# Performance work log

Hardware: AMD Instinct MI355X
Metric: run time of the kernel (lower is better)

## Reference

```python
import jax, jax.numpy as jnp
import numpy as np

N_EMBD = 2048
N_Q = 32
N_KV = 8
GROUP = N_Q // N_KV   # 4
HD = N_EMBD // N_Q    # 64
BASE = 10000.0
NEG_INF = -1e30


def _rope(x):
    """Rotate-half RoPE on last dim; positions 1..t along dim -2 (as in the
    original _build_cache which uses arange(1, seq_len+1))."""
    t, d = x.shape[-2], x.shape[-1]
    d2 = d // 2
    theta = 1.0 / (BASE ** (jnp.arange(0, d, 2, dtype=jnp.float32) / d))  # (d/2,)
    pos = jnp.arange(1, t + 1, dtype=jnp.float32)                          # (t,)
    ang = pos[:, None] * theta[None, :]                                    # (t, d/2)
    ang = jnp.concatenate([ang, ang], axis=-1)                             # (t, d)
    sin, cos = jnp.sin(ang), jnp.cos(ang)
    rot = jnp.concatenate([-x[..., d2:], x[..., :d2]], axis=-1)
    return x * cos + rot * sin


def setup_inputs() -> dict:
    key = jax.random.key(0)
    ks = jax.random.split(key, 5)
    b, t = 2, 1024
    s = 1.0 / np.sqrt(N_EMBD)
    return {
        "x": jax.random.normal(ks[0], (b, t, N_EMBD), dtype=jnp.float32),
        "wq": jax.random.normal(ks[1], (N_EMBD, N_EMBD), dtype=jnp.float32) * s,
        "bq": jnp.zeros((N_EMBD,), dtype=jnp.float32),
        "wk": jax.random.normal(ks[2], (N_EMBD, N_KV * HD), dtype=jnp.float32) * s,
        "bk": jnp.zeros((N_KV * HD,), dtype=jnp.float32),
        "wv": jax.random.normal(ks[3], (N_EMBD, N_KV * HD), dtype=jnp.float32) * s,
        "bv": jnp.zeros((N_KV * HD,), dtype=jnp.float32),
        "wo": jax.random.normal(ks[4], (N_EMBD, N_EMBD), dtype=jnp.float32) * s,
        "bo": jnp.zeros((N_EMBD,), dtype=jnp.float32),
    }


def reference(x, wq, bq, wk, bk, wv, bv, wo, bo):
    b, t, _ = x.shape
    q = x @ wq + bq                                   # (b, t, E)
    k = x @ wk + bk                                   # (b, t, NKV*HD)
    v = x @ wv + bv
    q = q.reshape(b, t, N_Q, HD).transpose(0, 2, 1, 3)        # (b, nq, t, d)
    q = q.reshape(b, N_KV, GROUP, t, HD)                      # (b, hkv, g, t, d)
    k = k.reshape(b, t, N_KV, HD).transpose(0, 2, 1, 3)       # (b, hkv, t, d)
    v = v.reshape(b, t, N_KV, HD).transpose(0, 2, 1, 3)
    q = _rope(q)
    k = _rope(k)
    scale = jnp.sqrt(jnp.float32(HD))
    att = jnp.einsum("bhgqd,bhkd->bhgqk", q, k) / scale       # (b, hkv, g, t, t)
    causal = jnp.tril(jnp.ones((t, t), dtype=bool))
    att = jnp.where(causal, att, NEG_INF)
    att = jax.nn.softmax(att, axis=-1)
    out = jnp.einsum("bhgqk,bhkd->bhgqd", att, v)             # (b, hkv, g, t, d)
    out = out.transpose(0, 3, 1, 2, 4).reshape(b, t, N_EMBD)  # (b, t, E)
    return out @ wo + bo
```

## Files before the change

kernel.cpp:

```cpp
#include <hip/hip_runtime.h>
#include <hip/hip_bf16.h>
#include <cstdint>


typedef __attribute__((ext_vector_type(8))) short short8;
typedef __attribute__((ext_vector_type(4))) short short4v;
typedef __attribute__((ext_vector_type(4))) float f32x4;

__device__ inline short f2b(float f) {
  union { float f; unsigned u; } v; v.f = f;
  unsigned r = v.u + 0x7fffu + ((v.u >> 16) & 1u);
  return (short)(r >> 16);
}

__device__ inline float exp2_fast(float x) {
  float r;
  asm("v_exp_f32 %0, %1" : "=v"(r) : "v"(x));
  return r;
}

__device__ inline void gl_lds16(const void* g, void* l) {
  __builtin_amdgcn_global_load_lds((const __attribute__((address_space(1))) void*)g,
                                   (__attribute__((address_space(3))) void*)l,
                                   16, 0, 0);
}

__global__ void cast_x_kernel(const float* __restrict__ x, short* __restrict__ xb, int n4) {
  int i = blockIdx.x * 256 + threadIdx.x;
  if (i >= n4) return;
  float4 v = ((const float4*)x)[i];
  short4v o; o.x = f2b(v.x); o.y = f2b(v.y); o.z = f2b(v.z); o.w = f2b(v.w);
  ((short4v*)xb)[i] = o;
}

__global__ void wtrans_all(const float* __restrict__ wq, const float* __restrict__ wk,
                           const float* __restrict__ wv, const float* __restrict__ wo,
                           short* __restrict__ WqkvT, short* __restrict__ woT) {
  __shared__ float tile[64][65];
  const int bx = blockIdx.x;
  const float* W; short* WT; int N, off, nb;
  if (bx < 32)      { W = wq; WT = WqkvT; N = 2048; off = 0;    nb = bx * 64; }
  else if (bx < 40) { W = wk; WT = WqkvT; N = 512;  off = 2048; nb = (bx - 32) * 64; }
  else if (bx < 48) { W = wv; WT = WqkvT; N = 512;  off = 2560; nb = (bx - 40) * 64; }
  else              { W = wo; WT = woT;   N = 2048; off = 0;    nb = (bx - 48) * 64; }
  const int kb = blockIdx.y * 64;
  const int tid = threadIdx.x;
  const int c = tid & 63, r0 = tid >> 6;
#pragma unroll
  for (int s = 0; s < 16; ++s) {
    int k = r0 + s * 4;
    tile[c][k] = W[(size_t)(kb + k) * N + nb + c];
  }
  __syncthreads();
#pragma unroll
  for (int s = 0; s < 16; ++s) {
    int n = r0 + s * 4;
    WT[(size_t)(off + nb + n) * 2048 + kb + c] = f2b(tile[n][c]);
  }
}

__device__ __forceinline__ void gemm_loop_bk64(const short* __restrict__ Ag,
                                               const short* __restrict__ Bg,
                                               short* lA, short* lB,
                                               int w, int l15, int q4,
                                               f32x4 acc[2][4]) {
  const int K = 2048, NS = 32;
  auto stage = [&](int s, int d) {
    const short* As = Ag + s * 64;
    const short* Bs = Bg + s * 64;
    short* a = lA + d * 8192 + w * 512;
    gl_lds16(As, a);
    gl_lds16(As + 64 * K, a + 2048);
    gl_lds16(As + 32, a + 4096);
    gl_lds16(As + 64 * K + 32, a + 6144);
    short* bp = lB + d * 4096 + w * 512;
    gl_lds16(Bs, bp);
    gl_lds16(Bs + 32, bp + 2048);
  };
  stage(0, 0);
  for (int s = 0; s < NS; ++s) {
    const int d = s & 1;
    __syncthreads();
    if (s + 1 < NS) stage(s + 1, d ^ 1);
#pragma unroll
    for (int ks = 0; ks < 2; ++ks) {
      const short* ap = lA + d * 8192 + ks * 4096;
      const short* bp = lB + d * 4096 + ks * 2048;
      short8 af[2], bf[4];
#pragma unroll
      for (int mf = 0; mf < 2; ++mf) af[mf] = *(const short8*)(ap + (w * 32 + mf * 16 + l15) * 32 + q4 * 8);
#pragma unroll
      for (int nf = 0; nf < 4; ++nf) bf[nf] = *(const short8*)(bp + (nf * 16 + l15) * 32 + q4 * 8);
#pragma unroll
      for (int mf = 0; mf < 2; ++mf)
#pragma unroll
        for (int nf = 0; nf < 4; ++nf)
          acc[mf][nf] = __builtin_amdgcn_mfma_f32_16x16x32_bf16(af[mf], bf[nf], acc[mf][nf], 0, 0, 0);
    }
  }
}

__launch_bounds__(256, 3)
__global__ void gemm_qkv(const short* __restrict__ A, const short* __restrict__ BT,
                         const float* __restrict__ bq, const float* __restrict__ bk,
                         const float* __restrict__ bv,
                         short* __restrict__ Qb, short* __restrict__ Kb,
                         short* __restrict__ Vtd) {
  __shared__ __align__(16) short lA[16384];
  __shared__ __align__(16) short lB[8192];
  const int K = 2048;
  const int tid = threadIdx.x, lane = tid & 63, w = tid >> 6;
  const int q4 = lane >> 4, l15 = lane & 15;
  const int bn = blockIdx.x * 64, bm = blockIdx.y * 128;

  const short* Ag = A + (size_t)(bm + (tid >> 2)) * K + ((tid & 3) << 3);
  const short* Bg = BT + (size_t)(bn + (tid >> 2)) * K + ((tid & 3) << 3);

  f32x4 acc[2][4];
  const f32x4 fz = {0.f, 0.f, 0.f, 0.f};
#pragma unroll
  for (int i = 0; i < 2; ++i)
#pragma unroll
    for (int j = 0; j < 4; ++j) acc[i][j] = fz;

  gemm_loop_bk64(Ag, Bg, lA, lB, w, l15, q4, acc);

  const float L2T = 0.4152410118609203f;
  const float theta_a = exp2_fast(-(float)l15 * L2T);
  const float theta_b = exp2_fast(-(float)(l15 + 16) * L2T);
  const float s2 = 0.18033688011112042f;

  if (bn < 2048) {
    const int h = bn >> 6;
    float bb0 = bq[bn + l15], bb1 = bq[bn + 16 + l15], bb2 = bq[bn + 32 + l15], bb3 = bq[bn + 48 + l15];
#pragma unroll
    for (int mf = 0; mf < 2; ++mf)
#pragma unroll
      for (int r = 0; r < 4; ++r) {
        int row = bm + w * 32 + mf * 16 + q4 * 4 + r;
        int batch = row >> 10, t = row & 1023;
        float pos = (float)(t + 1);
        float sa, ca, sb, cb;
        __sincosf(pos * theta_a, &sa, &ca);
        __sincosf(pos * theta_b, &sb, &cb);
        float x0 = acc[mf][0][r] + bb0, x2 = acc[mf][2][r] + bb2;
        float x1 = acc[mf][1][r] + bb1, x3 = acc[mf][3][r] + bb3;
        size_t base = ((size_t)(batch * 32 + h) * 1024 + t) * 64;
        Qb[base + l15]      = f2b((x0 * ca - x2 * sa) * s2);
        Qb[base + l15 + 32] = f2b((x2 * ca + x0 * sa) * s2);
        Qb[base + l15 + 16] = f2b((x1 * cb - x3 * sb) * s2);
        Qb[base + l15 + 48] = f2b((x3 * cb + x1 * sb) * s2);
      }
  } else if (bn < 2560) {
    const int co = bn - 2048;
    const int hkv = co >> 6;
    float bb0 = bk[co + l15], bb1 = bk[co + 16 + l15], bb2 = bk[co + 32 + l15], bb3 = bk[co + 48 + l15];
#pragma unroll
    for (int mf = 0; mf < 2; ++mf)
#pragma unroll
      for (int r = 0; r < 4; ++r) {
        int row = bm + w * 32 + mf * 16 + q4 * 4 + r;
        int batch = row >> 10, t = row & 1023;
        float pos = (float)(t + 1);
        float sa, ca, sb, cb;
        __sincosf(pos * theta_a, &sa, &ca);
        __sincosf(pos * theta_b, &sb, &cb);
        float x0 = acc[mf][0][r] + bb0, x2 = acc[mf][2][r] + bb2;
        float x1 = acc[mf][1][r] + bb1, x3 = acc[mf][3][r] + bb3;
        size_t base = (size_t)(batch * 8 + hkv) * 65536 + t * 32;
        Kb[base + l15]              = f2b(x0 * ca - x2 * sa);
        Kb[base + l15 + 16]         = f2b(x1 * cb - x3 * sb);
        Kb[base + 32768 + l15]      = f2b(x2 * ca + x0 * sa);
        Kb[base + 32768 + l15 + 16] = f2b(x3 * cb + x1 * sb);
      }
  } else {
    const int co = bn - 2560;
    const int hkv = co >> 6;
    float bb[4];
#pragma unroll
    for (int nf = 0; nf < 4; ++nf) bb[nf] = bv[co + nf * 16 + l15];
#pragma unroll
    for (int mf = 0; mf < 2; ++mf)
#pragma unroll
      for (int r = 0; r < 4; ++r) {
        int row = bm + w * 32 + mf * 16 + q4 * 4 + r;
        int batch = row >> 10, t = row & 1023;
        size_t base = (size_t)(batch * 8 + hkv) * 65536 + (size_t)t * 64;
#pragma unroll
        for (int nf = 0; nf < 4; ++nf)
          Vtd[base + nf * 16 + l15] = f2b(acc[mf][nf][r] + bb[nf]);
      }
  }
}

__global__ void vtrans2_kernel(const short* __restrict__ Vtd, short* __restrict__ VTb) {
  __shared__ short tile[64][72];
  const int tt = blockIdx.x, h = blockIdx.y, b = blockIdx.z;
  const int tid = threadIdx.x;
  const size_t base = (size_t)(b * 8 + h) * 65536;
#pragma unroll
  for (int p = 0; p < 2; ++p) {
    int r = (tid >> 3) + p * 32;
    int c0 = (tid & 7) * 8;
    short8 v = *(const short8*)(Vtd + base + (size_t)(tt * 64 + r) * 64 + c0);
#pragma unroll
    for (int j = 0; j < 8; ++j) tile[c0 + j][r] = v[j];
  }
  __syncthreads();
  const int d = tid >> 2, ts = (tid & 3) * 8;
#pragma unroll
  for (int tc = 0; tc < 2; ++tc) {
    short8 v = *(const short8*)(&tile[d][tc * 32 + ts]);
    *(short8*)(VTb + base + (size_t)(tt * 2 + tc) * 2048 + d * 32 + ts) = v;
  }
}

#define PROW 72
__launch_bounds__(256, 3)
__global__ void attn5_kernel(const short* __restrict__ Qb, const short* __restrict__ Kb,
                             const short* __restrict__ VTb, short* __restrict__ AO) {
  __shared__ __align__(16) short lK[2][128 * 32];
  __shared__ __align__(16) short lVT[4][64 * 32];
  __shared__ __align__(16) short lP[4][2][16 * PROW];
  const int tid = threadIdx.x, lane = tid & 63, w = tid >> 6;
  const int q4 = lane >> 4, l15 = lane & 15;
  const int qt = (int)gridDim.x - 1 - (int)blockIdx.x;
  const int h = blockIdx.y, b = blockIdx.z;
  const int hkv = h >> 2;
  const int qb = qt * 128 + w * 32;
  const int kdiag = qb >> 6;
  const int ns = qt + 1;

  const short* Qg = Qb + (size_t)(b * 32 + h) * 65536;
  const short* Kg = Kb + (size_t)(b * 8 + hkv) * 65536;
  const short* Vg = VTb + (size_t)(b * 8 + hkv) * 65536;

  short8 qf[2][2];
#pragma unroll
  for (int mf = 0; mf < 2; ++mf) {
    const short* qr = Qg + (size_t)(qb + mf * 16 + l15) * 64 + q4 * 8;
    qf[mf][0] = *(const short8*)(qr);
    qf[mf][1] = *(const short8*)(qr + 32);
  }

  const f32x4 fz = {0.f, 0.f, 0.f, 0.f};
  f32x4 o[2][4], ol[2];
#pragma unroll
  for (int mf = 0; mf < 2; ++mf) {
    ol[mf] = fz;
#pragma unroll
    for (int i = 0; i < 4; ++i) o[mf][i] = fz;
  }
  short8 ones;
#pragma unroll
  for (int i = 0; i < 8; ++i) ones[i] = (short)0x3F80;

  for (int s = 0; s < ns; ++s) {
    {
      const short* Ksrc = Kg + (size_t)(s * 128 + (tid >> 2)) * 32 + (tid & 3) * 8;
      short* ldst = (short*)lK + w * 512;
      gl_lds16(Ksrc, ldst);
      gl_lds16(Ksrc + 64 * 32, ldst + 2048);
      gl_lds16(Ksrc + 32768, ldst + 4096);
      gl_lds16(Ksrc + 32768 + 64 * 32, ldst + 6144);
      const short* Vsrc = Vg + (size_t)(s * 4) * 2048 + tid * 8;
      short* vdst = (short*)lVT + w * 512;
#pragma unroll
      for (int c = 0; c < 4; ++c) gl_lds16(Vsrc + c * 2048, vdst + c * 2048);
    }
    __syncthreads();

#pragma unroll
    for (int ki = 0; ki < 2; ++ki) {
      const int ktg = s * 2 + ki;
      if (ktg <= kdiag) {
        short8 kf0[4], kf1[4];
#pragma unroll
        for (int nt = 0; nt < 4; ++nt) {
          kf0[nt] = *(const short8*)((short*)lK + (ki * 64 + nt * 16 + l15) * 32 + q4 * 8);
          kf1[nt] = *(const short8*)((short*)lK + 4096 + (ki * 64 + nt * 16 + l15) * 32 + q4 * 8);
        }
        const bool diag = (ktg == kdiag);
#pragma unroll
        for (int mf = 0; mf < 2; ++mf) {
          f32x4 sv[4];
#pragma unroll
          for (int nt = 0; nt < 4; ++nt) {
            f32x4 z = __builtin_amdgcn_mfma_f32_16x16x32_bf16(qf[mf][0], kf0[nt], fz, 0, 0, 0);
            sv[nt] = __builtin_amdgcn_mfma_f32_16x16x32_bf16(qf[mf][1], kf1[nt], z, 0, 0, 0);
          }
          if (diag) {
#pragma unroll
            for (int r = 0; r < 4; ++r) {
              const int qrow = qb + mf * 16 + q4 * 4 + r;
              const int col = ktg * 64 + l15;
#pragma unroll
              for (int nt = 0; nt < 4; ++nt)
                if (col + nt * 16 > qrow) sv[nt][r] = -1e30f;
            }
          }
          short* lPm = lP[w][mf];
#pragma unroll
          for (int r = 0; r < 4; ++r)
#pragma unroll
            for (int nt = 0; nt < 4; ++nt)
              lPm[(q4 * 4 + r) * PROW + nt * 16 + l15] = f2b(exp2_fast(sv[nt][r] - 16.f));
        }

        short8 vf0[4], vf1[4];
#pragma unroll
        for (int dt = 0; dt < 4; ++dt) {
          vf0[dt] = *(const short8*)((short*)lVT + (2 * ki) * 2048 + (dt * 16 + l15) * 32 + q4 * 8);
          vf1[dt] = *(const short8*)((short*)lVT + (2 * ki + 1) * 2048 + (dt * 16 + l15) * 32 + q4 * 8);
        }
#pragma unroll
        for (int mf = 0; mf < 2; ++mf) {
          const short* lPm = lP[w][mf];
          short8 pf0 = *(const short8*)(lPm + l15 * PROW + q4 * 8);
          short8 pf1 = *(const short8*)(lPm + l15 * PROW + 32 + q4 * 8);
          ol[mf] = __builtin_amdgcn_mfma_f32_16x16x32_bf16(pf0, ones, ol[mf], 0, 0, 0);
          ol[mf] = __builtin_amdgcn_mfma_f32_16x16x32_bf16(pf1, ones, ol[mf], 0, 0, 0);
#pragma unroll
          for (int dt = 0; dt < 4; ++dt) {
            o[mf][dt] = __builtin_amdgcn_mfma_f32_16x16x32_bf16(pf0, vf0[dt], o[mf][dt], 0, 0, 0);
            o[mf][dt] = __builtin_amdgcn_mfma_f32_16x16x32_bf16(pf1, vf1[dt], o[mf][dt], 0, 0, 0);
          }
        }
      }
    }
    __syncthreads();
  }

#pragma unroll
  for (int mf = 0; mf < 2; ++mf)
#pragma unroll
    for (int r = 0; r < 4; ++r) {
      float inv = __builtin_amdgcn_rcpf(ol[mf][r]);
      int row = qb + mf * 16 + q4 * 4 + r;
#pragma unroll
      for (int dt = 0; dt < 4; ++dt)
        AO[(size_t)(b * 1024 + row) * 2048 + h * 64 + dt * 16 + l15] = f2b(o[mf][dt][r] * inv);
    }
}

__launch_bounds__(256, 3)
__global__ void gemm_out(const short* __restrict__ A, const short* __restrict__ BT,
                         float* __restrict__ C, const float* __restrict__ bias,
                         int N, int K) {
  __shared__ __align__(16) short lA[16384];
  __shared__ __align__(16) short lB[8192];
  const int tid = threadIdx.x, lane = tid & 63, w = tid >> 6;
  const int q4 = lane >> 4, l15 = lane & 15;
  const int bn = blockIdx.x * 64, bm = blockIdx.y * 128;

  const short* Ag = A + (size_t)(bm + (tid >> 2)) * K + ((tid & 3) << 3);
  const short* Bg = BT + (size_t)(bn + (tid >> 2)) * K + ((tid & 3) << 3);

  f32x4 acc[2][4];
  const f32x4 fz = {0.f, 0.f, 0.f, 0.f};
#pragma unroll
  for (int i = 0; i < 2; ++i)
#pragma unroll
    for (int j = 0; j < 4; ++j) acc[i][j] = fz;

  gemm_loop_bk64(Ag, Bg, lA, lB, w, l15, q4, acc);

#pragma unroll
  for (int mf = 0; mf < 2; ++mf)
#pragma unroll
    for (int nf = 0; nf < 4; ++nf) {
      int col = bn + nf * 16 + l15;
      float bb = bias[col];
#pragma unroll
      for (int r = 0; r < 4; ++r) {
        int row = bm + w * 32 + mf * 16 + q4 * 4 + r;
        C[(size_t)row * N + col] = acc[mf][nf][r] + bb;
      }
    }
}

extern "C" void kernel_launch(void* const* d_in, const int* in_sizes, int n_in,
                              void* d_out, int out_size, void* d_ws, size_t ws_size,
                              hipStream_t stream) {
  const float* x  = (const float*)d_in[0];
  const float* wq = (const float*)d_in[1];
  const float* bq = (const float*)d_in[2];
  const float* wk = (const float*)d_in[3];
  const float* bk = (const float*)d_in[4];
  const float* wv = (const float*)d_in[5];
  const float* bv = (const float*)d_in[6];
  const float* wo = (const float*)d_in[7];
  const float* bo = (const float*)d_in[8];
  float* out = (float*)d_out;
  const int B = in_sizes[0] / (1024 * 2048);
  const int M = B * 1024;

  char* ws = (char*)d_ws;
  size_t off = 0;
  auto alloc = [&](size_t bytes) -> char* {
    char* p = ws + off;
    off += (bytes + 255) & ~(size_t)255;
    return p;
  };
  short* xb    = (short*)alloc((size_t)M * 2048 * 2);
  short* WqkvT = (short*)alloc((size_t)3072 * 2048 * 2);
  short* woT   = (short*)alloc((size_t)2048 * 2048 * 2);
  short* Qb    = (short*)alloc((size_t)B * 32 * 1024 * 64 * 2);
  short* Kb    = (short*)alloc((size_t)B * 8 * 2 * 1024 * 32 * 2);
  short* Vtd   = (short*)alloc((size_t)B * 8 * 1024 * 64 * 2);
  short* VTb   = (short*)alloc((size_t)B * 8 * 32 * 64 * 32 * 2);
  short* AO    = (short*)alloc((size_t)M * 2048 * 2);

  cast_x_kernel<<<(M * 2048 / 4 + 255) / 256, 256, 0, stream>>>(x, xb, M * 2048 / 4);
  wtrans_all<<<dim3(80, 32), 256, 0, stream>>>(wq, wk, wv, wo, WqkvT, woT);
  gemm_qkv<<<dim3(48, M / 128), 256, 0, stream>>>(xb, WqkvT, bq, bk, bv, Qb, Kb, Vtd);
  vtrans2_kernel<<<dim3(16, 8, B), 256, 0, stream>>>(Vtd, VTb);
  attn5_kernel<<<dim3(8, 32, B), 256, 0, stream>>>(Qb, Kb, VTb, AO);
  gemm_out<<<dim3(32, M / 128), 256, 0, stream>>>(AO, woT, out, bo, 2048, 2048);
}
```

Baseline: 208.7 us.

## Swizzle LDS layouts and deepen GEMM pipeline to four-stage half-tile ring

The GEMM main loop moves from a double-buffered BK=64 schedule to a four-slot ring of BK=32 half-steps with three loads in flight. Each step waits with explicit vmcnt counts and a raw s_barrier instead of __syncthreads, and MFMA priority is raised with s_setprio. The source column offsets of the global-to-LDS copies and the fragment read offsets are XOR-swizzled in both the GEMMs and the attention kernel, to cut LDS bank conflicts on the short8 reads. The hand-counted vmcnt values and the swizzle must match the copy pattern exactly, or the results go wrong.

New measurement: 226.3 us. 8.4% more time.

```diff
diff --git a/kernel.cpp b/kernel.cpp
--- a/kernel.cpp
+++ b/kernel.cpp
@@ -64,40 +64,59 @@
                                                short* lA, short* lB,
                                                int w, int l15, int q4,
                                                f32x4 acc[2][4]) {
-  const int K = 2048, NS = 32;
-  auto stage = [&](int s, int d) {
-    const short* As = Ag + s * 64;
-    const short* Bs = Bg + s * 64;
-    short* a = lA + d * 8192 + w * 512;
+  const int K = 2048, HS = 64;
+  const int q4x = q4 ^ ((l15 >> 1) & 3);
+
+  auto issue = [&](int h) {
+    const short* As = Ag + h * 32;
+    const short* Bs = Bg + h * 32;
+    const int be = h & 3;
+    short* a = lA + be * 4096 + w * 512;
     gl_lds16(As, a);
     gl_lds16(As + 64 * K, a + 2048);
-    gl_lds16(As + 32, a + 4096);
-    gl_lds16(As + 64 * K + 32, a + 6144);
-    short* bp = lB + d * 4096 + w * 512;
-    gl_lds16(Bs, bp);
-    gl_lds16(Bs + 32, bp + 2048);
+    gl_lds16(Bs, lB + be * 2048 + w * 512);
   };
-  stage(0, 0);
-  for (int s = 0; s < NS; ++s) {
-    const int d = s & 1;
-    __syncthreads();
-    if (s + 1 < NS) stage(s + 1, d ^ 1);
-#pragma unroll
-    for (int ks = 0; ks < 2; ++ks) {
-      const short* ap = lA + d * 8192 + ks * 4096;
-      const short* bp = lB + d * 4096 + ks * 2048;
-      short8 af[2], bf[4];
-#pragma unroll
-      for (int mf = 0; mf < 2; ++mf) af[mf] = *(const short8*)(ap + (w * 32 + mf * 16 + l15) * 32 + q4 * 8);
-#pragma unroll
-      for (int nf = 0; nf < 4; ++nf) bf[nf] = *(const short8*)(bp + (nf * 16 + l15) * 32 + q4 * 8);
-#pragma unroll
-      for (int mf = 0; mf < 2; ++mf)
-#pragma unroll
-        for (int nf = 0; nf < 4; ++nf)
-          acc[mf][nf] = __builtin_amdgcn_mfma_f32_16x16x32_bf16(af[mf], bf[nf], acc[mf][nf], 0, 0, 0);
-    }
-  }
+  auto halfstep = [&](int h) {
+    const int be = h & 3;
+    const short* ap = lA + be * 4096;
+    const short* bp = lB + be * 2048;
+    short8 af[2], bf[4];
+#pragma unroll
+    for (int mf = 0; mf < 2; ++mf)
+      af[mf] = *(const short8*)(ap + (w * 32 + mf * 16 + l15) * 32 + q4x * 8);
+#pragma unroll
+    for (int nf = 0; nf < 4; ++nf)
+      bf[nf] = *(const short8*)(bp + (nf * 16 + l15) * 32 + q4x * 8);
+    __builtin_amdgcn_s_setprio(1);
+#pragma unroll
+    for (int mf = 0; mf < 2; ++mf)
+#pragma unroll
+      for (int nf = 0; nf < 4; ++nf)
+        acc[mf][nf] = __builtin_amdgcn_mfma_f32_16x16x32_bf16(af[mf], bf[nf], acc[mf][nf], 0, 0, 0);
+    __builtin_amdgcn_s_setprio(0);
+  };
+
+  issue(0); issue(1); issue(2);
+  for (int h = 0; h < HS - 3; ++h) {
+    asm volatile("s_waitcnt vmcnt(6)" ::: "memory");
+    __builtin_amdgcn_s_barrier();
+    asm volatile("" ::: "memory");
+    __builtin_amdgcn_sched_barrier(0);
+    issue(h + 3);
+    halfstep(h);
+  }
+  asm volatile("s_waitcnt vmcnt(6)" ::: "memory");
+  __builtin_amdgcn_s_barrier();
+  asm volatile("" ::: "memory");
+  halfstep(HS - 3);
+  asm volatile("s_waitcnt vmcnt(3)" ::: "memory");
+  __builtin_amdgcn_s_barrier();
+  asm volatile("" ::: "memory");
+  halfstep(HS - 2);
+  asm volatile("s_waitcnt vmcnt(0)" ::: "memory");
+  __builtin_amdgcn_s_barrier();
+  asm volatile("" ::: "memory");
+  halfstep(HS - 1);
 }
 
 __launch_bounds__(256, 3)
@@ -113,8 +132,9 @@
   const int q4 = lane >> 4, l15 = lane & 15;
   const int bn = blockIdx.x * 64, bm = blockIdx.y * 128;
 
-  const short* Ag = A + (size_t)(bm + (tid >> 2)) * K + ((tid & 3) << 3);
-  const short* Bg = BT + (size_t)(bn + (tid >> 2)) * K + ((tid & 3) << 3);
+  const int swzc = ((tid & 3) ^ ((tid >> 3) & 3)) << 3;
+  const short* Ag = A + (size_t)(bm + (tid >> 2)) * K + swzc;
+  const short* Bg = BT + (size_t)(bn + (tid >> 2)) * K + swzc;
 
   f32x4 acc[2][4];
   const f32x4 fz = {0.f, 0.f, 0.f, 0.f};
@@ -224,6 +244,8 @@
   __shared__ __align__(16) short lP[4][2][16 * PROW];
   const int tid = threadIdx.x, lane = tid & 63, w = tid >> 6;
   const int q4 = lane >> 4, l15 = lane & 15;
+  const int q4x = q4 ^ ((l15 >> 1) & 3);
+  const int swzc = ((tid & 3) ^ ((tid >> 3) & 3)) << 3;
   const int qt = (int)gridDim.x - 1 - (int)blockIdx.x;
   const int h = blockIdx.y, b = blockIdx.z;
   const int hkv = h >> 2;
@@ -257,13 +279,13 @@
 
   for (int s = 0; s < ns; ++s) {
     {
-      const short* Ksrc = Kg + (size_t)(s * 128 + (tid >> 2)) * 32 + (tid & 3) * 8;
+      const short* Ksrc = Kg + (size_t)(s * 128 + (tid >> 2)) * 32 + swzc;
       short* ldst = (short*)lK + w * 512;
       gl_lds16(Ksrc, ldst);
       gl_lds16(Ksrc + 64 * 32, ldst + 2048);
       gl_lds16(Ksrc + 32768, ldst + 4096);
       gl_lds16(Ksrc + 32768 + 64 * 32, ldst + 6144);
-      const short* Vsrc = Vg + (size_t)(s * 4) * 2048 + tid * 8;
+      const short* Vsrc = Vg + (size_t)(s * 4) * 2048 + (tid >> 2) * 32 + swzc;
       short* vdst = (short*)lVT + w * 512;
 #pragma unroll
       for (int c = 0; c < 4; ++c) gl_lds16(Vsrc + c * 2048, vdst + c * 2048);
@@ -277,8 +299,8 @@
         short8 kf0[4], kf1[4];
 #pragma unroll
         for (int nt = 0; nt < 4; ++nt) {
-          kf0[nt] = *(const short8*)((short*)lK + (ki * 64 + nt * 16 + l15) * 32 + q4 * 8);
-          kf1[nt] = *(const short8*)((short*)lK + 4096 + (ki * 64 + nt * 16 + l15) * 32 + q4 * 8);
+          kf0[nt] = *(const short8*)((short*)lK + (ki * 64 + nt * 16 + l15) * 32 + q4x * 8);
+          kf1[nt] = *(const short8*)((short*)lK + 4096 + (ki * 64 + nt * 16 + l15) * 32 + q4x * 8);
         }
         const bool diag = (ktg == kdiag);
 #pragma unroll
@@ -310,8 +332,8 @@
         short8 vf0[4], vf1[4];
 #pragma unroll
         for (int dt = 0; dt < 4; ++dt) {
-          vf0[dt] = *(const short8*)((short*)lVT + (2 * ki) * 2048 + (dt * 16 + l15) * 32 + q4 * 8);
-          vf1[dt] = *(const short8*)((short*)lVT + (2 * ki + 1) * 2048 + (dt * 16 + l15) * 32 + q4 * 8);
+          vf0[dt] = *(const short8*)((short*)lVT + (2 * ki) * 2048 + (dt * 16 + l15) * 32 + q4x * 8);
+          vf1[dt] = *(const short8*)((short*)lVT + (2 * ki + 1) * 2048 + (dt * 16 + l15) * 32 + q4x * 8);
         }
 #pragma unroll
         for (int mf = 0; mf < 2; ++mf) {
@@ -353,8 +375,9 @@
   const int q4 = lane >> 4, l15 = lane & 15;
   const int bn = blockIdx.x * 64, bm = blockIdx.y * 128;
 
-  const short* Ag = A + (size_t)(bm + (tid >> 2)) * K + ((tid & 3) << 3);
-  const short* Bg = BT + (size_t)(bn + (tid >> 2)) * K + ((tid & 3) << 3);
+  const int swzc = ((tid & 3) ^ ((tid >> 3) & 3)) << 3;
+  const short* Ag = A + (size_t)(bm + (tid >> 2)) * K + swzc;
+  const short* Bg = BT + (size_t)(bn + (tid >> 2)) * K + swzc;
 
   f32x4 acc[2][4];
   const f32x4 fz = {0.f, 0.f, 0.f, 0.f};
```

## Use 128x128 GEMM tiles with 2x2 wave layout and XOR-swizzled LDS

Applied to the files above, without the earlier changes.

The QKV and output projection GEMMs move from 128x64 tiles with BK=64 to 128x128 tiles with BK=32. Each wave now computes a 64x64 sub-tile, which raises arithmetic intensity and halves the number of blocks. An XOR swizzle on the 16-byte column chunk is applied to both the global-to-LDS loads and the fragment reads, in the GEMMs and in the attention K/V tiles, to cut LDS bank conflicts. The cost is more accumulator registers, fewer blocks (grids of 24x16 and 16x16 on a large GPU, so lower occupancy), and twice as many K-loop iterations with a barrier each.

Result: slower. 225.7 us (+8.1%).

```diff
diff --git a/kernel.cpp b/kernel.cpp
--- a/kernel.cpp
+++ b/kernel.cpp
@@ -59,44 +59,42 @@
   }
 }
 
-__device__ __forceinline__ void gemm_loop_bk64(const short* __restrict__ Ag,
-                                               const short* __restrict__ Bg,
-                                               short* lA, short* lB,
-                                               int w, int l15, int q4,
-                                               f32x4 acc[2][4]) {
-  const int K = 2048, NS = 32;
+__device__ __forceinline__ void gemm_loop_128(const short* __restrict__ Ag,
+                                              const short* __restrict__ Bg,
+                                              short* lA, short* lB,
+                                              int w, int wr, int wc, int l15, int q4,
+                                              f32x4 acc[4][4]) {
+  const int K = 2048, NS = 64;
+  const int q4x = q4 ^ ((l15 >> 1) & 3);
+
   auto stage = [&](int s, int d) {
-    const short* As = Ag + s * 64;
-    const short* Bs = Bg + s * 64;
-    short* a = lA + d * 8192 + w * 512;
-    gl_lds16(As, a);
-    gl_lds16(As + 64 * K, a + 2048);
-    gl_lds16(As + 32, a + 4096);
-    gl_lds16(As + 64 * K + 32, a + 6144);
-    short* bp = lB + d * 4096 + w * 512;
-    gl_lds16(Bs, bp);
-    gl_lds16(Bs + 32, bp + 2048);
+    const short* As = Ag + s * 32;
+    const short* Bs = Bg + s * 32;
+    gl_lds16(As,          lA + d * 4096 + w * 512);
+    gl_lds16(As + 64 * K, lA + d * 4096 + 2048 + w * 512);
+    gl_lds16(Bs,          lB + d * 4096 + w * 512);
+    gl_lds16(Bs + 64 * K, lB + d * 4096 + 2048 + w * 512);
   };
+
   stage(0, 0);
   for (int s = 0; s < NS; ++s) {
     const int d = s & 1;
     __syncthreads();
     if (s + 1 < NS) stage(s + 1, d ^ 1);
-#pragma unroll
-    for (int ks = 0; ks < 2; ++ks) {
-      const short* ap = lA + d * 8192 + ks * 4096;
-      const short* bp = lB + d * 4096 + ks * 2048;
-      short8 af[2], bf[4];
-#pragma unroll
-      for (int mf = 0; mf < 2; ++mf) af[mf] = *(const short8*)(ap + (w * 32 + mf * 16 + l15) * 32 + q4 * 8);
-#pragma unroll
-      for (int nf = 0; nf < 4; ++nf) bf[nf] = *(const short8*)(bp + (nf * 16 + l15) * 32 + q4 * 8);
-#pragma unroll
-      for (int mf = 0; mf < 2; ++mf)
-#pragma unroll
-        for (int nf = 0; nf < 4; ++nf)
-          acc[mf][nf] = __builtin_amdgcn_mfma_f32_16x16x32_bf16(af[mf], bf[nf], acc[mf][nf], 0, 0, 0);
-    }
+    const short* ap = lA + d * 4096;
+    const short* bp = lB + d * 4096;
+    short8 af[4], bf[4];
+#pragma unroll
+    for (int mi = 0; mi < 4; ++mi)
+      af[mi] = *(const short8*)(ap + (wr * 64 + mi * 16 + l15) * 32 + q4x * 8);
+#pragma unroll
+    for (int ni = 0; ni < 4; ++ni)
+      bf[ni] = *(const short8*)(bp + (wc * 64 + ni * 16 + l15) * 32 + q4x * 8);
+#pragma unroll
+    for (int mi = 0; mi < 4; ++mi)
+#pragma unroll
+      for (int ni = 0; ni < 4; ++ni)
+        acc[mi][ni] = __builtin_amdgcn_mfma_f32_16x16x32_bf16(af[mi], bf[ni], acc[mi][ni], 0, 0, 0);
   }
 }
 
@@ -106,89 +104,92 @@
                          const float* __restrict__ bv,
                          short* __restrict__ Qb, short* __restrict__ Kb,
                          short* __restrict__ Vtd) {
-  __shared__ __align__(16) short lA[16384];
+  __shared__ __align__(16) short lA[8192];
   __shared__ __align__(16) short lB[8192];
   const int K = 2048;
   const int tid = threadIdx.x, lane = tid & 63, w = tid >> 6;
+  const int wr = w >> 1, wc = w & 1;
   const int q4 = lane >> 4, l15 = lane & 15;
-  const int bn = blockIdx.x * 64, bm = blockIdx.y * 128;
-
-  const short* Ag = A + (size_t)(bm + (tid >> 2)) * K + ((tid & 3) << 3);
-  const short* Bg = BT + (size_t)(bn + (tid >> 2)) * K + ((tid & 3) << 3);
-
-  f32x4 acc[2][4];
+  const int bn = blockIdx.x * 128, bm = blockIdx.y * 128;
+
+  const int swzc = ((tid & 3) ^ ((tid >> 3) & 3)) << 3;
+  const short* Ag = A + (size_t)(bm + (tid >> 2)) * K + swzc;
+  const short* Bg = BT + (size_t)(bn + (tid >> 2)) * K + swzc;
+
+  f32x4 acc[4][4];
   const f32x4 fz = {0.f, 0.f, 0.f, 0.f};
 #pragma unroll
-  for (int i = 0; i < 2; ++i)
+  for (int i = 0; i < 4; ++i)
 #pragma unroll
     for (int j = 0; j < 4; ++j) acc[i][j] = fz;
 
-  gemm_loop_bk64(Ag, Bg, lA, lB, w, l15, q4, acc);
+  gemm_loop_128(Ag, Bg, lA, lB, w, wr, wc, l15, q4, acc);
 
   const float L2T = 0.4152410118609203f;
   const float theta_a = exp2_fast(-(float)l15 * L2T);
   const float theta_b = exp2_fast(-(float)(l15 + 16) * L2T);
   const float s2 = 0.18033688011112042f;
-
-  if (bn < 2048) {
-    const int h = bn >> 6;
-    float bb0 = bq[bn + l15], bb1 = bq[bn + 16 + l15], bb2 = bq[bn + 32 + l15], bb3 = bq[bn + 48 + l15];
-#pragma unroll
-    for (int mf = 0; mf < 2; ++mf)
+  const int cb = bn + wc * 64;
+
+  if (cb < 2048) {
+    const int h = cb >> 6;
+    float bb0 = bq[cb + l15], bb1 = bq[cb + 16 + l15], bb2 = bq[cb + 32 + l15], bb3 = bq[cb + 48 + l15];
+#pragma unroll
+    for (int mi = 0; mi < 4; ++mi)
 #pragma unroll
       for (int r = 0; r < 4; ++r) {
-        int row = bm + w * 32 + mf * 16 + q4 * 4 + r;
+        int row = bm + wr * 64 + mi * 16 + q4 * 4 + r;
         int batch = row >> 10, t = row & 1023;
         float pos = (float)(t + 1);
-        float sa, ca, sb, cb;
+        float sa, ca, sb, cb2;
         __sincosf(pos * theta_a, &sa, &ca);
-        __sincosf(pos * theta_b, &sb, &cb);
-        float x0 = acc[mf][0][r] + bb0, x2 = acc[mf][2][r] + bb2;
-        float x1 = acc[mf][1][r] + bb1, x3 = acc[mf][3][r] + bb3;
+        __sincosf(pos * theta_b, &sb, &cb2);
+        float x0 = acc[mi][0][r] + bb0, x2 = acc[mi][2][r] + bb2;
+        float x1 = acc[mi][1][r] + bb1, x3 = acc[mi][3][r] + bb3;
         size_t base = ((size_t)(batch * 32 + h) * 1024 + t) * 64;
         Qb[base + l15]      = f2b((x0 * ca - x2 * sa) * s2);
         Qb[base + l15 + 32] = f2b((x2 * ca + x0 * sa) * s2);
-        Qb[base + l15 + 16] = f2b((x1 * cb - x3 * sb) * s2);
-        Qb[base + l15 + 48] = f2b((x3 * cb + x1 * sb) * s2);
+        Qb[base + l15 + 16] = f2b((x1 * cb2 - x3 * sb) * s2);
+        Qb[base + l15 + 48] = f2b((x3 * cb2 + x1 * sb) * s2);
       }
-  } else if (bn < 2560) {
-    const int co = bn - 2048;
+  } else if (cb < 2560) {
+    const int co = cb - 2048;
     const int hkv = co >> 6;
     float bb0 = bk[co + l15], bb1 = bk[co + 16 + l15], bb2 = bk[co + 32 + l15], bb3 = bk[co + 48 + l15];
 #pragma unroll
-    for (int mf = 0; mf < 2; ++mf)
+    for (int mi = 0; mi < 4; ++mi)
 #pragma unroll
       for (int r = 0; r < 4; ++r) {
-        int row = bm + w * 32 + mf * 16 + q4 * 4 + r;
+        int row = bm + wr * 64 + mi * 16 + q4 * 4 + r;
         int batch = row >> 10, t = row & 1023;
         float pos = (float)(t + 1);
-        float sa, ca, sb, cb;
+        float sa, ca, sb, cb2;
         __sincosf(pos * theta_a, &sa, &ca);
-        __sincosf(pos * theta_b, &sb, &cb);
-        float x0 = acc[mf][0][r] + bb0, x2 = acc[mf][2][r] + bb2;
-        float x1 = acc[mf][1][r] + bb1, x3 = acc[mf][3][r] + bb3;
+        __sincosf(pos * theta_b, &sb, &cb2);
+        float x0 = acc[mi][0][r] + bb0, x2 = acc[mi][2][r] + bb2;
+        float x1 = acc[mi][1][r] + bb1, x3 = acc[mi][3][r] + bb3;
         size_t base = (size_t)(batch * 8 + hkv) * 65536 + t * 32;
         Kb[base + l15]              = f2b(x0 * ca - x2 * sa);
-        Kb[base + l15 + 16]         = f2b(x1 * cb - x3 * sb);
+        Kb[base + l15 + 16]         = f2b(x1 * cb2 - x3 * sb);
         Kb[base + 32768 + l15]      = f2b(x2 * ca + x0 * sa);
-        Kb[base + 32768 + l15 + 16] = f2b(x3 * cb + x1 * sb);
+        Kb[base + 32768 + l15 + 16] = f2b(x3 * cb2 + x1 * sb);
       }
   } else {
-    const int co = bn - 2560;
+    const int co = cb - 2560;
     const int hkv = co >> 6;
     float bb[4];
 #pragma unroll
     for (int nf = 0; nf < 4; ++nf) bb[nf] = bv[co + nf * 16 + l15];
 #pragma unroll
-    for (int mf = 0; mf < 2; ++mf)
+    for (int mi = 0; mi < 4; ++mi)
 #pragma unroll
       for (int r = 0; r < 4; ++r) {
-        int row = bm + w * 32 + mf * 16 + q4 * 4 + r;
+        int row = bm + wr * 64 + mi * 16 + q4 * 4 + r;
         int batch = row >> 10, t = row & 1023;
         size_t base = (size_t)(batch * 8 + hkv) * 65536 + (size_t)t * 64;
 #pragma unroll
         for (int nf = 0; nf < 4; ++nf)
-          Vtd[base + nf * 16 + l15] = f2b(acc[mf][nf][r] + bb[nf]);
+          Vtd[base + nf * 16 + l15] = f2b(acc[mi][nf][r] + bb[nf]);
       }
   }
 }
@@ -224,6 +225,8 @@
   __shared__ __align__(16) short lP[4][2][16 * PROW];
   const int tid = threadIdx.x, lane = tid & 63, w = tid >> 6;
   const int q4 = lane >> 4, l15 = lane & 15;
+  const int q4x = q4 ^ ((l15 >> 1) & 3);
+  const int swzc = ((tid & 3) ^ ((tid >> 3) & 3)) << 3;
   const int qt = (int)gridDim.x - 1 - (int)blockIdx.x;
   const int h = blockIdx.y, b = blockIdx.z;
   const int hkv = h >> 2;
@@ -257,13 +260,13 @@
 
   for (int s = 0; s < ns; ++s) {
     {
-      const short* Ksrc = Kg + (size_t)(s * 128 + (tid >> 2)) * 32 + (tid & 3) * 8;
+      const short* Ksrc = Kg + (size_t)(s * 128 + (tid >> 2)) * 32 + swzc;
       short* ldst = (short*)lK + w * 512;
       gl_lds16(Ksrc, ldst);
       gl_lds16(Ksrc + 64 * 32, ldst + 2048);
       gl_lds16(Ksrc + 32768, ldst + 4096);
       gl_lds16(Ksrc + 32768 + 64 * 32, ldst + 6144);
-      const short* Vsrc = Vg + (size_t)(s * 4) * 2048 + tid * 8;
+      const short* Vsrc = Vg + (size_t)(s * 4) * 2048 + (tid >> 2) * 32 + swzc;
       short* vdst = (short*)lVT + w * 512;
 #pragma unroll
       for (int c = 0; c < 4; ++c) gl_lds16(Vsrc + c * 2048, vdst + c * 2048);
@@ -277,8 +280,8 @@
         short8 kf0[4], kf1[4];
 #pragma unroll
         for (int nt = 0; nt < 4; ++nt) {
-          kf0[nt] = *(const short8*)((short*)lK + (ki * 64 + nt * 16 + l15) * 32 + q4 * 8);
-          kf1[nt] = *(const short8*)((short*)lK + 4096 + (ki * 64 + nt * 16 + l15) * 32 + q4 * 8);
+          kf0[nt] = *(const short8*)((short*)lK + (ki * 64 + nt * 16 + l15) * 32 + q4x * 8);
+          kf1[nt] = *(const short8*)((short*)lK + 4096 + (ki * 64 + nt * 16 + l15) * 32 + q4x * 8);
         }
         const bool diag = (ktg == kdiag);
 #pragma unroll
@@ -310,8 +313,8 @@
         short8 vf0[4], vf1[4];
 #pragma unroll
         for (int dt = 0; dt < 4; ++dt) {
-          vf0[dt] = *(const short8*)((short*)lVT + (2 * ki) * 2048 + (dt * 16 + l15) * 32 + q4 * 8);
-          vf1[dt] = *(const short8*)((short*)lVT + (2 * ki + 1) * 2048 + (dt * 16 + l15) * 32 + q4 * 8);
+          vf0[dt] = *(const short8*)((short*)lVT + (2 * ki) * 2048 + (dt * 16 + l15) * 32 + q4x * 8);
+          vf1[dt] = *(const short8*)((short*)lVT + (2 * ki + 1) * 2048 + (dt * 16 + l15) * 32 + q4x * 8);
         }
 #pragma unroll
         for (int mf = 0; mf < 2; ++mf) {
@@ -347,34 +350,36 @@
 __global__ void gemm_out(const short* __restrict__ A, const short* __restrict__ BT,
                          float* __restrict__ C, const float* __restrict__ bias,
                          int N, int K) {
-  __shared__ __align__(16) short lA[16384];
+  __shared__ __align__(16) short lA[8192];
   __shared__ __align__(16) short lB[8192];
   const int tid = threadIdx.x, lane = tid & 63, w = tid >> 6;
+  const int wr = w >> 1, wc = w & 1;
   const int q4 = lane >> 4, l15 = lane & 15;
-  const int bn = blockIdx.x * 64, bm = blockIdx.y * 128;
-
-  const short* Ag = A + (size_t)(bm + (tid >> 2)) * K + ((tid & 3) << 3);
-  const short* Bg = BT + (size_t)(bn + (tid >> 2)) * K + ((tid & 3) << 3);
-
-  f32x4 acc[2][4];
+  const int bn = blockIdx.x * 128, bm = blockIdx.y * 128;
+
+  const int swzc = ((tid & 3) ^ ((tid >> 3) & 3)) << 3;
+  const short* Ag = A + (size_t)(bm + (tid >> 2)) * K + swzc;
+  const short* Bg = BT + (size_t)(bn + (tid >> 2)) * K + swzc;
+
+  f32x4 acc[4][4];
   const f32x4 fz = {0.f, 0.f, 0.f, 0.f};
 #pragma unroll
-  for (int i = 0; i < 2; ++i)
+  for (int i = 0; i < 4; ++i)
 #pragma unroll
     for (int j = 0; j < 4; ++j) acc[i][j] = fz;
 
-  gemm_loop_bk64(Ag, Bg, lA, lB, w, l15, q4, acc);
-
-#pragma unroll
-  for (int mf = 0; mf < 2; ++mf)
-#pragma unroll
-    for (int nf = 0; nf < 4; ++nf) {
-      int col = bn + nf * 16 + l15;
+  gemm_loop_128(Ag, Bg, lA, lB, w, wr, wc, l15, q4, acc);
+
+#pragma unroll
+  for (int mi = 0; mi < 4; ++mi)
+#pragma unroll
+    for (int ni = 0; ni < 4; ++ni) {
+      int col = bn + wc * 64 + ni * 16 + l15;
       float bb = bias[col];
 #pragma unroll
       for (int r = 0; r < 4; ++r) {
-        int row = bm + w * 32 + mf * 16 + q4 * 4 + r;
-        C[(size_t)row * N + col] = acc[mf][nf][r] + bb;
+        int row = bm + wr * 64 + mi * 16 + q4 * 4 + r;
+        C[(size_t)row * N + col] = acc[mi][ni][r] + bb;
       }
     }
 }
@@ -413,8 +418,8 @@
 
   cast_x_kernel<<<(M * 2048 / 4 + 255) / 256, 256, 0, stream>>>(x, xb, M * 2048 / 4);
   wtrans_all<<<dim3(80, 32), 256, 0, stream>>>(wq, wk, wv, wo, WqkvT, woT);
-  gemm_qkv<<<dim3(48, M / 128), 256, 0, stream>>>(xb, WqkvT, bq, bk, bv, Qb, Kb, Vtd);
+  gemm_qkv<<<dim3(24, M / 128), 256, 0, stream>>>(xb, WqkvT, bq, bk, bv, Qb, Kb, Vtd);
   vtrans2_kernel<<<dim3(16, 8, B), 256, 0, stream>>>(Vtd, VTb);
   attn5_kernel<<<dim3(8, 32, B), 256, 0, stream>>>(Qb, Kb, VTb, AO);
-  gemm_out<<<dim3(32, M / 128), 256, 0, stream>>>(AO, woT, out, bo, 2048, 2048);
-}
+  gemm_out<<<dim3(16, M / 128), 256, 0, stream>>>(AO, woT, out, bo, 2048, 2048);
+}
```

## Swizzle LDS tiles to avoid bank conflicts and fuse V transpose into QKV GEMM

Applied to the files above, without the earlier changes.

Applies an XOR swizzle to the 16-byte chunk index both when global-to-LDS loads write tiles and when MFMA fragments are read back, in the GEMM loop and the attention kernel. This is meant to cut LDS bank conflicts on the fragment reads. The QKV GEMM epilogue now writes V straight into the transposed blocked layout that attention consumes, as packed 4-element stores, so the separate vtrans2 kernel and its intermediate buffer go away. The cost is slightly more index arithmetic and less coalesced V stores.

New measurement: 206.2 us. About the same (-1.2%).

```diff
diff --git a/kernel.cpp b/kernel.cpp
--- a/kernel.cpp
+++ b/kernel.cpp
@@ -65,6 +65,7 @@
                                                int w, int l15, int q4,
                                                f32x4 acc[2][4]) {
   const int K = 2048, NS = 32;
+  const int q4x = q4 ^ ((l15 >> 1) & 3);
   auto stage = [&](int s, int d) {
     const short* As = Ag + s * 64;
     const short* Bs = Bg + s * 64;
@@ -88,9 +89,9 @@
       const short* bp = lB + d * 4096 + ks * 2048;
       short8 af[2], bf[4];
 #pragma unroll
-      for (int mf = 0; mf < 2; ++mf) af[mf] = *(const short8*)(ap + (w * 32 + mf * 16 + l15) * 32 + q4 * 8);
-#pragma unroll
-      for (int nf = 0; nf < 4; ++nf) bf[nf] = *(const short8*)(bp + (nf * 16 + l15) * 32 + q4 * 8);
+      for (int mf = 0; mf < 2; ++mf) af[mf] = *(const short8*)(ap + (w * 32 + mf * 16 + l15) * 32 + q4x * 8);
+#pragma unroll
+      for (int nf = 0; nf < 4; ++nf) bf[nf] = *(const short8*)(bp + (nf * 16 + l15) * 32 + q4x * 8);
 #pragma unroll
       for (int mf = 0; mf < 2; ++mf)
 #pragma unroll
@@ -105,7 +106,7 @@
                          const float* __restrict__ bq, const float* __restrict__ bk,
                          const float* __restrict__ bv,
                          short* __restrict__ Qb, short* __restrict__ Kb,
-                         short* __restrict__ Vtd) {
+                         short* __restrict__ VTb) {
   __shared__ __align__(16) short lA[16384];
   __shared__ __align__(16) short lB[8192];
   const int K = 2048;
@@ -113,8 +114,9 @@
   const int q4 = lane >> 4, l15 = lane & 15;
   const int bn = blockIdx.x * 64, bm = blockIdx.y * 128;
 
-  const short* Ag = A + (size_t)(bm + (tid >> 2)) * K + ((tid & 3) << 3);
-  const short* Bg = BT + (size_t)(bn + (tid >> 2)) * K + ((tid & 3) << 3);
+  const int swzc = ((tid & 3) ^ ((tid >> 3) & 3)) << 3;
+  const short* Ag = A + (size_t)(bm + (tid >> 2)) * K + swzc;
+  const short* Bg = BT + (size_t)(bn + (tid >> 2)) * K + swzc;
 
   f32x4 acc[2][4];
   const f32x4 fz = {0.f, 0.f, 0.f, 0.f};
@@ -179,39 +181,20 @@
     float bb[4];
 #pragma unroll
     for (int nf = 0; nf < 4; ++nf) bb[nf] = bv[co + nf * 16 + l15];
-#pragma unroll
-    for (int mf = 0; mf < 2; ++mf)
-#pragma unroll
-      for (int r = 0; r < 4; ++r) {
-        int row = bm + w * 32 + mf * 16 + q4 * 4 + r;
-        int batch = row >> 10, t = row & 1023;
-        size_t base = (size_t)(batch * 8 + hkv) * 65536 + (size_t)t * 64;
-#pragma unroll
-        for (int nf = 0; nf < 4; ++nf)
-          Vtd[base + nf * 16 + l15] = f2b(acc[mf][nf][r] + bb[nf]);
+    const int batch = (bm + w * 32) >> 10;
+    const size_t vbase = (size_t)(batch * 8 + hkv) * 65536;
+#pragma unroll
+    for (int mf = 0; mf < 2; ++mf) {
+      const int t0 = (bm + w * 32 + mf * 16 + q4 * 4) & 1023;
+      const size_t rbase = vbase + (size_t)(t0 >> 5) * 2048 + (t0 & 31);
+#pragma unroll
+      for (int nf = 0; nf < 4; ++nf) {
+        short4v pk;
+#pragma unroll
+        for (int r = 0; r < 4; ++r) pk[r] = f2b(acc[mf][nf][r] + bb[nf]);
+        *(short4v*)(VTb + rbase + (nf * 16 + l15) * 32) = pk;
       }
-  }
-}
-
-__global__ void vtrans2_kernel(const short* __restrict__ Vtd, short* __restrict__ VTb) {
-  __shared__ short tile[64][72];
-  const int tt = blockIdx.x, h = blockIdx.y, b = blockIdx.z;
-  const int tid = threadIdx.x;
-  const size_t base = (size_t)(b * 8 + h) * 65536;
-#pragma unroll
-  for (int p = 0; p < 2; ++p) {
-    int r = (tid >> 3) + p * 32;
-    int c0 = (tid & 7) * 8;
-    short8 v = *(const short8*)(Vtd + base + (size_t)(tt * 64 + r) * 64 + c0);
-#pragma unroll
-    for (int j = 0; j < 8; ++j) tile[c0 + j][r] = v[j];
-  }
-  __syncthreads();
-  const int d = tid >> 2, ts = (tid & 3) * 8;
-#pragma unroll
-  for (int tc = 0; tc < 2; ++tc) {
-    short8 v = *(const short8*)(&tile[d][tc * 32 + ts]);
-    *(short8*)(VTb + base + (size_t)(tt * 2 + tc) * 2048 + d * 32 + ts) = v;
+    }
   }
 }
 
@@ -224,6 +207,8 @@
   __shared__ __align__(16) short lP[4][2][16 * PROW];
   const int tid = threadIdx.x, lane = tid & 63, w = tid >> 6;
   const int q4 = lane >> 4, l15 = lane & 15;
+  const int q4x = q4 ^ ((l15 >> 1) & 3);
+  const int swzc = ((tid & 3) ^ ((tid >> 3) & 3)) << 3;
   const int qt = (int)gridDim.x - 1 - (int)blockIdx.x;
   const int h = blockIdx.y, b = blockIdx.z;
   const int hkv = h >> 2;
@@ -257,13 +242,13 @@
 
   for (int s = 0; s < ns; ++s) {
     {
-      const short* Ksrc = Kg + (size_t)(s * 128 + (tid >> 2)) * 32 + (tid & 3) * 8;
+      const short* Ksrc = Kg + (size_t)(s * 128 + (tid >> 2)) * 32 + swzc;
       short* ldst = (short*)lK + w * 512;
       gl_lds16(Ksrc, ldst);
       gl_lds16(Ksrc + 64 * 32, ldst + 2048);
       gl_lds16(Ksrc + 32768, ldst + 4096);
       gl_lds16(Ksrc + 32768 + 64 * 32, ldst + 6144);
-      const short* Vsrc = Vg + (size_t)(s * 4) * 2048 + tid * 8;
+      const short* Vsrc = Vg + (size_t)(s * 4) * 2048 + (tid >> 2) * 32 + swzc;
       short* vdst = (short*)lVT + w * 512;
 #pragma unroll
       for (int c = 0; c < 4; ++c) gl_lds16(Vsrc + c * 2048, vdst + c * 2048);
@@ -277,8 +262,8 @@
         short8 kf0[4], kf1[4];
 #pragma unroll
         for (int nt = 0; nt < 4; ++nt) {
-          kf0[nt] = *(const short8*)((short*)lK + (ki * 64 + nt * 16 + l15) * 32 + q4 * 8);
-          kf1[nt] = *(const short8*)((short*)lK + 4096 + (ki * 64 + nt * 16 + l15) * 32 + q4 * 8);
+          kf0[nt] = *(const short8*)((short*)lK + (ki * 64 + nt * 16 + l15) * 32 + q4x * 8);
+          kf1[nt] = *(const short8*)((short*)lK + 4096 + (ki * 64 + nt * 16 + l15) * 32 + q4x * 8);
         }
         const bool diag = (ktg == kdiag);
 #pragma unroll
@@ -310,8 +295,8 @@
         short8 vf0[4], vf1[4];
 #pragma unroll
         for (int dt = 0; dt < 4; ++dt) {
-          vf0[dt] = *(const short8*)((short*)lVT + (2 * ki) * 2048 + (dt * 16 + l15) * 32 + q4 * 8);
-          vf1[dt] = *(const short8*)((short*)lVT + (2 * ki + 1) * 2048 + (dt * 16 + l15) * 32 + q4 * 8);
+          vf0[dt] = *(const short8*)((short*)lVT + (2 * ki) * 2048 + (dt * 16 + l15) * 32 + q4x * 8);
+          vf1[dt] = *(const short8*)((short*)lVT + (2 * ki + 1) * 2048 + (dt * 16 + l15) * 32 + q4x * 8);
         }
 #pragma unroll
         for (int mf = 0; mf < 2; ++mf) {
@@ -353,8 +338,9 @@
   const int q4 = lane >> 4, l15 = lane & 15;
   const int bn = blockIdx.x * 64, bm = blockIdx.y * 128;
 
-  const short* Ag = A + (size_t)(bm + (tid >> 2)) * K + ((tid & 3) << 3);
-  const short* Bg = BT + (size_t)(bn + (tid >> 2)) * K + ((tid & 3) << 3);
+  const int swzc = ((tid & 3) ^ ((tid >> 3) & 3)) << 3;
+  const short* Ag = A + (size_t)(bm + (tid >> 2)) * K + swzc;
+  const short* Bg = BT + (size_t)(bn + (tid >> 2)) * K + swzc;
 
   f32x4 acc[2][4];
   const f32x4 fz = {0.f, 0.f, 0.f, 0.f};
@@ -407,14 +393,12 @@
   short* woT   = (short*)alloc((size_t)2048 * 2048 * 2);
   short* Qb    = (short*)alloc((size_t)B * 32 * 1024 * 64 * 2);
   short* Kb    = (short*)alloc((size_t)B * 8 * 2 * 1024 * 32 * 2);
-  short* Vtd   = (short*)alloc((size_t)B * 8 * 1024 * 64 * 2);
   short* VTb   = (short*)alloc((size_t)B * 8 * 32 * 64 * 32 * 2);
   short* AO    = (short*)alloc((size_t)M * 2048 * 2);
 
   cast_x_kernel<<<(M * 2048 / 4 + 255) / 256, 256, 0, stream>>>(x, xb, M * 2048 / 4);
   wtrans_all<<<dim3(80, 32), 256, 0, stream>>>(wq, wk, wv, wo, WqkvT, woT);
-  gemm_qkv<<<dim3(48, M / 128), 256, 0, stream>>>(xb, WqkvT, bq, bk, bv, Qb, Kb, Vtd);
-  vtrans2_kernel<<<dim3(16, 8, B), 256, 0, stream>>>(Vtd, VTb);
+  gemm_qkv<<<dim3(48, M / 128), 256, 0, stream>>>(xb, WqkvT, bq, bk, bv, Qb, Kb, VTb);
   attn5_kernel<<<dim3(8, 32, B), 256, 0, stream>>>(Qb, Kb, VTb, AO);
   gemm_out<<<dim3(32, M / 128), 256, 0, stream>>>(AO, woT, out, bo, 2048, 2048);
 }
```
